# Kernel tuning notes

Measured on AMD Instinct MI355X. Metric: run time of the kernel, lower is better.

Reference implementation:

```python
import jax, jax.numpy as jnp
import numpy as np

B, S, H, NH = 2, 2048, 2048, 16
HD = H // NH  # 128
ROPE_BASE = 10000.0


def _rope(q, k, position_ids):
    # q, k: [B, NH, S, HD]; position_ids: [B, S]
    half = HD // 2
    inv_freq = 1.0 / (ROPE_BASE ** (jnp.arange(0, half, dtype=jnp.float32) / half))
    freqs = position_ids.astype(jnp.float32)[:, :, None] * inv_freq[None, None, :]  # [B,S,half]
    emb = jnp.concatenate([freqs, freqs], axis=-1)                                   # [B,S,HD]
    cos = jnp.cos(emb)[:, None, :, :]  # [B,1,S,HD]
    sin = jnp.sin(emb)[:, None, :, :]

    def rot_half(x):
        x1, x2 = jnp.split(x, 2, axis=-1)
        return jnp.concatenate([-x2, x1], axis=-1)

    q = q * cos + rot_half(q) * sin
    k = k * cos + rot_half(k) * sin
    return q, k


def setup_inputs() -> dict:
    key = jax.random.key(0)
    k1, k2, k3 = jax.random.split(key, 3)
    hidden_states = jax.random.normal(k1, (B, S, H), dtype=jnp.float32)
    position_ids = jnp.broadcast_to(jnp.arange(S, dtype=jnp.int32), (B, S))
    # additive causal mask (large finite negative to avoid inf arithmetic)
    causal = jnp.triu(jnp.full((S, S), -1e9, dtype=jnp.float32), k=1)
    attention_mask = jnp.broadcast_to(causal[None, None], (B, 1, S, S))
    qkv_w = jax.random.normal(k2, (3 * H, H), dtype=jnp.float32) * (H ** -0.5)
    qkv_b = jnp.zeros((3 * H,), dtype=jnp.float32)
    o_w = jax.random.normal(k3, (H, H), dtype=jnp.float32) * (H ** -0.5)
    return {"hidden_states": hidden_states, "position_ids": position_ids,
            "attention_mask": attention_mask, "qkv_w": qkv_w, "qkv_b": qkv_b, "o_w": o_w}


def reference(hidden_states, position_ids, attention_mask, qkv_w, qkv_b, o_w):
    qkv = hidden_states @ qkv_w.T + qkv_b                      # [B,S,3H]
    q, k, v = jnp.split(qkv, 3, axis=-1)

    def to_heads(x):
        return x.reshape(B, S, NH, HD).transpose(0, 2, 1, 3)   # [B,NH,S,HD]

    q, k, v = to_heads(q), to_heads(k), to_heads(v)
    q, k = _rope(q, k, position_ids)

    scale = 1.0 / np.sqrt(HD)
    scores = jnp.einsum('bhqd,bhkd->bhqk', q, k * scale)
    scores = scores + attention_mask
    probs = jax.nn.softmax(scores.astype(jnp.float32), axis=-1).astype(q.dtype)
    attn = jnp.einsum('bhqk,bhkd->bhqd', probs, v)
    attn = attn.transpose(0, 2, 1, 3).reshape(B, S, H)
    return attn @ o_w.T
```

## Files before the change

### kernel.cpp

```cpp
#include <hip/hip_runtime.h>
#include <hip/hip_bf16.h>

#define BB 2
#define SS 2048
#define HH 2048
#define NHH 16
#define HDD 128

using f32x4  = __attribute__((ext_vector_type(4))) float;
using bf16x8 = __attribute__((ext_vector_type(8))) short;

__device__ __forceinline__ unsigned short f2bf(float x) {
  unsigned int u = __float_as_uint(x);
  unsigned int r = (u + 0x7FFFu + ((u >> 16) & 1u)) >> 16;
  return (unsigned short)r;
}
__device__ __forceinline__ float bf2f(unsigned short u) {
  return __uint_as_float(((unsigned int)u) << 16);
}

__device__ __forceinline__ void gll16(const void* g, void* l) {
  __builtin_amdgcn_global_load_lds(
      (__attribute__((address_space(1))) void*)(g),
      (__attribute__((address_space(3))) void*)(l), 16, 0, 0);
}

#define MFMA16(a, b, c) __builtin_amdgcn_mfma_f32_16x16x32_bf16(a, b, c, 0, 0, 0)

template<int N> __device__ __forceinline__ void wlgkm() {
  static_assert(N == 0 || N == 2 || N == 4 || N == 6 || N == 8 || N == 10 || N == 12,
                "unsupported lgkmcnt");
  if constexpr (N == 0)       asm volatile("s_waitcnt lgkmcnt(0)"  ::: "memory");
  else if constexpr (N == 2)  asm volatile("s_waitcnt lgkmcnt(2)"  ::: "memory");
  else if constexpr (N == 4)  asm volatile("s_waitcnt lgkmcnt(4)"  ::: "memory");
  else if constexpr (N == 6)  asm volatile("s_waitcnt lgkmcnt(6)"  ::: "memory");
  else if constexpr (N == 8)  asm volatile("s_waitcnt lgkmcnt(8)"  ::: "memory");
  else if constexpr (N == 10) asm volatile("s_waitcnt lgkmcnt(10)" ::: "memory");
  else if constexpr (N == 12) asm volatile("s_waitcnt lgkmcnt(12)" ::: "memory");
}
template<int N> __device__ __forceinline__ void wvm() {
  static_assert(N == 0 || N == 5 || N == 6 || N == 7 || N == 8, "unsupported vmcnt");
  if constexpr (N == 0)      asm volatile("s_waitcnt vmcnt(0)" ::: "memory");
  else if constexpr (N == 5) asm volatile("s_waitcnt vmcnt(5)" ::: "memory");
  else if constexpr (N == 6) asm volatile("s_waitcnt vmcnt(6)" ::: "memory");
  else if constexpr (N == 7) asm volatile("s_waitcnt vmcnt(7)" ::: "memory");
  else if constexpr (N == 8) asm volatile("s_waitcnt vmcnt(8)" ::: "memory");
}


__global__ void convert_bf16(const float* __restrict__ in, unsigned short* __restrict__ out, int n4) {
  int i = blockIdx.x * blockDim.x + threadIdx.x;
  if (i >= n4) return;
  float4 v = reinterpret_cast<const float4*>(in)[i];
  ushort4 o;
  o.x = f2bf(v.x); o.y = f2bf(v.y); o.z = f2bf(v.z); o.w = f2bf(v.w);
  reinterpret_cast<ushort4*>(out)[i] = o;
}

__global__ void build_tab(float* __restrict__ tab) {
  int i = blockIdx.x * blockDim.x + threadIdx.x;
  if (i >= SS * 64) return;
  int s = i >> 6, j = i & 63;
  float invf = expf(-logf(10000.f) * ((float)j / 64.f));
  float a = (float)s * invf;
  tab[i * 2]     = cosf(a);
  tab[i * 2 + 1] = sinf(a);
}


template<int MODE, int MI>
__global__ __launch_bounds__(512, 1)
void gemm_pipe(const unsigned short* __restrict__ A,
               const unsigned short* __restrict__ Bw,
               const float* __restrict__ bias,
               float* __restrict__ outF,
               unsigned short* __restrict__ outQ,
               unsigned short* __restrict__ outK,
               unsigned short* __restrict__ outV,
               int Kdim) {
  constexpr int BM = 32 * MI;
  __shared__ unsigned short lA[2][BM * 64];
  __shared__ unsigned short lB[2][256 * 64];
  const int tid = threadIdx.x;
  const int tn = blockIdx.x, tm = blockIdx.y;
  const int wid = tid >> 6, lane = tid & 63;
  const int wm = wid >> 2, wn = wid & 3;
  const int lr = lane & 15, lg = lane >> 4;

  const unsigned short* Ab = A + (size_t)tm * BM * Kdim;
  const unsigned short* Bb = Bw + (size_t)tn * 256 * Kdim;

  f32x4 acc[MI][4] = {};
  bf16x8 af[MI][2], bfr[4][2];

  const int nt = Kdim >> 6;

  auto stageA = [&](int t, int h) {
    unsigned short* L = lA[t & 1];
    const int k0 = t << 6;
#pragma unroll
    for (int p = 0; p < BM / 128; ++p) {
      int cl = p * 512 + tid;
      int ri = cl >> 3, c = cl & 7;
      int row = (ri / (8 * MI)) * (16 * MI) + h * (8 * MI) + (ri % (8 * MI));
      int cg = c ^ (row & 7);
      gll16(Ab + (size_t)row * Kdim + k0 + (cg << 3), L + row * 64 + (c << 3));
    }
  };
  auto stageB = [&](int t, int h) {
    unsigned short* L = lB[t & 1];
    const int k0 = t << 6;
#pragma unroll
    for (int p = 0; p < 2; ++p) {
      int cl = p * 512 + tid;
      int ri = cl >> 3, c = cl & 7;
      int row = (ri >> 5 << 6) + (h << 5) + (ri & 31);
      int cg = c ^ (row & 7);
      gll16(Bb + (size_t)row * Kdim + k0 + (cg << 3), L + row * 64 + (c << 3));
    }
  };
  auto readAhalf = [&](int g, int h) {
    const unsigned short* la = lA[g & 1];
#pragma unroll
    for (int mi = h * (MI / 2); mi < (h + 1) * (MI / 2); ++mi) {
      int ra = wm * (BM / 2) + mi * 16 + lr;
      af[mi][0] = *reinterpret_cast<const bf16x8*>(la + ra * 64 + ((lg ^ (ra & 7)) << 3));
      af[mi][1] = *reinterpret_cast<const bf16x8*>(la + ra * 64 + (((4 + lg) ^ (ra & 7)) << 3));
    }
  };
  auto readBhalf = [&](int g, int h) {
    const unsigned short* lb = lB[g & 1];
#pragma unroll
    for (int ni = h * 2; ni < h * 2 + 2; ++ni) {
      int rb = wn * 64 + ni * 16 + lr;
      bfr[ni][0] = *reinterpret_cast<const bf16x8*>(lb + rb * 64 + ((lg ^ (rb & 7)) << 3));
      bfr[ni][1] = *reinterpret_cast<const bf16x8*>(lb + rb * 64 + (((4 + lg) ^ (rb & 7)) << 3));
    }
  };
  auto quad = [&](int ah, int bh) {
    __builtin_amdgcn_s_setprio(1);
#pragma unroll
    for (int mi = ah * (MI / 2); mi < (ah + 1) * (MI / 2); ++mi)
#pragma unroll
      for (int ni = bh * 2; ni < bh * 2 + 2; ++ni) {
        acc[mi][ni] = MFMA16(af[mi][0], bfr[ni][0], acc[mi][ni]);
        acc[mi][ni] = MFMA16(af[mi][1], bfr[ni][1], acc[mi][ni]);
      }
    __builtin_amdgcn_s_setprio(0);
  };

  stageA(0, 0); stageA(0, 1); stageB(0, 0); stageB(0, 1);
  stageA(1, 0); stageA(1, 1); stageB(1, 0); stageB(1, 1);
  if constexpr (MI == 8) wvm<8>();
  else                   wvm<6>();
  __builtin_amdgcn_s_barrier();
  __builtin_amdgcn_sched_barrier(0);
  readAhalf(0, 0);
  readBhalf(0, 0);

  for (int g = 0; g < nt; ++g) {
    readBhalf(g, 1);
    wlgkm<4>();
    __builtin_amdgcn_sched_barrier(0);
    quad(0, 0);

    readAhalf(g, 1);
    if constexpr (MI == 8) wlgkm<8>(); else wlgkm<4>();
    __builtin_amdgcn_sched_barrier(0);
    quad(0, 1);

    asm volatile("s_waitcnt vmcnt(0) lgkmcnt(0)" ::: "memory");
    __builtin_amdgcn_s_barrier();
    __builtin_amdgcn_sched_barrier(0);
    if (g + 1 < nt) readAhalf(g + 1, 0);
    if (g + 2 < nt) { stageA(g + 2, 0); stageA(g + 2, 1); }
    quad(1, 0);

    if (g + 1 < nt) readBhalf(g + 1, 0);
    if (g + 2 < nt) { stageB(g + 2, 0); stageB(g + 2, 1); }
    quad(1, 1);
  }

#pragma unroll
  for (int mi = 0; mi < MI; ++mi) {
#pragma unroll
    for (int ni = 0; ni < 4; ++ni) {
      int n = tn * 256 + wn * 64 + ni * 16 + lr;
#pragma unroll
      for (int r = 0; r < 4; ++r) {
        int m = tm * BM + wm * (BM / 2) + mi * 16 + lg * 4 + r;
        float v = acc[mi][ni][r];
        if (MODE == 1) {
          v += bias[n];
          int sel = n >> 11;
          int h = (n >> 7) & 15;
          int d = n & 127;
          int b = m >> 11;
          int s = m & 2047;
          if (sel == 0)
            outQ[(((size_t)(b * 16 + h)) * 2048 + s) * 128 + d] = f2bf(v);
          else if (sel == 1)
            outK[(((size_t)(b * 16 + h)) * 2048 + s) * 128 + d] = f2bf(v);
          else
            outV[(((size_t)(b * 16 + h)) * 128 + d) * 2048 + s] = f2bf(v);
        } else {
          outF[(size_t)m * 2048 + n] = v;
        }
      }
    }
  }
}


template<int MODE>
__global__ __launch_bounds__(256)
void gemm97(const unsigned short* __restrict__ A,
            const unsigned short* __restrict__ Bw,
            const float* __restrict__ bias,
            float* __restrict__ outF,
            unsigned short* __restrict__ outQ,
            unsigned short* __restrict__ outK,
            unsigned short* __restrict__ outV,
            int Kdim) {
  __shared__ unsigned short lA[128 * 64];
  __shared__ unsigned short lB[128 * 64];
  const int tid = threadIdx.x;
  const int tn = blockIdx.x, tm = blockIdx.y;
  const int wid = tid >> 6, lane = tid & 63;
  const int wm = wid >> 1, wn = wid & 1;
  const int lr = lane & 15, lg = lane >> 4;

  const unsigned short* Ab = A + (size_t)tm * 128 * Kdim;
  const unsigned short* Bb = Bw + (size_t)tn * 128 * Kdim;

  f32x4 acc[4][4] = {};

  const unsigned short* sa[4];
  const unsigned short* sb[4];
  unsigned short* da[4];
  unsigned short* db[4];
#pragma unroll
  for (int p = 0; p < 4; ++p) {
    int cl = p * 256 + tid;
    int ri = cl >> 3, c = cl & 7;
    int cg = c ^ (ri & 7);
    sa[p] = Ab + (size_t)ri * Kdim + (cg << 3);
    sb[p] = Bb + (size_t)ri * Kdim + (cg << 3);
    da[p] = lA + ri * 64 + (c << 3);
    db[p] = lB + ri * 64 + (c << 3);
  }

  const int nt = Kdim >> 6;

  for (int k = 0; k < nt; ++k) {
#pragma unroll
    for (int p = 0; p < 4; ++p) {
      gll16(sa[p], da[p]); sa[p] += 64;
      gll16(sb[p], db[p]); sb[p] += 64;
    }
    __syncthreads();

    bf16x8 af[4][2], bf[4][2];
#pragma unroll
    for (int t = 0; t < 4; ++t) {
      int ra = wm * 64 + t * 16 + lr;
      int rb = wn * 64 + t * 16 + lr;
      af[t][0] = *reinterpret_cast<const bf16x8*>(lA + ra * 64 + ((lg ^ (ra & 7)) << 3));
      af[t][1] = *reinterpret_cast<const bf16x8*>(lA + ra * 64 + (((4 + lg) ^ (ra & 7)) << 3));
      bf[t][0] = *reinterpret_cast<const bf16x8*>(lB + rb * 64 + ((lg ^ (rb & 7)) << 3));
      bf[t][1] = *reinterpret_cast<const bf16x8*>(lB + rb * 64 + (((4 + lg) ^ (rb & 7)) << 3));
    }
#pragma unroll
    for (int i = 0; i < 4; ++i)
#pragma unroll
      for (int j = 0; j < 4; ++j) {
        acc[i][j] = MFMA16(af[i][0], bf[j][0], acc[i][j]);
        acc[i][j] = MFMA16(af[i][1], bf[j][1], acc[i][j]);
      }
    __syncthreads();
  }

#pragma unroll
  for (int i = 0; i < 4; ++i) {
#pragma unroll
    for (int j = 0; j < 4; ++j) {
      int n = tn * 128 + wn * 64 + j * 16 + lr;
#pragma unroll
      for (int r = 0; r < 4; ++r) {
        int m = tm * 128 + wm * 64 + i * 16 + lg * 4 + r;
        float v = acc[i][j][r];
        if (MODE == 1) {
          v += bias[n];
          int sel = n >> 11;
          int h = (n >> 7) & 15;
          int d = n & 127;
          int b = m >> 11;
          int s = m & 2047;
          if (sel == 0)
            outQ[(((size_t)(b * 16 + h)) * 2048 + s) * 128 + d] = f2bf(v);
          else if (sel == 1)
            outK[(((size_t)(b * 16 + h)) * 2048 + s) * 128 + d] = f2bf(v);
          else
            outV[(((size_t)(b * 16 + h)) * 128 + d) * 2048 + s] = f2bf(v);
        } else {
          outF[(size_t)m * 2048 + n] = v;
        }
      }
    }
  }
}


__global__ void rope_inplace(unsigned short* __restrict__ Qr, unsigned short* __restrict__ Kr,
                             const int* __restrict__ pos, const float* __restrict__ tab) {
  int i = blockIdx.x * blockDim.x + threadIdx.x;
  if (i >= (1 << 20)) return;
  int jb = i & 7;
  int s  = (i >> 3) & 2047;
  int bh = (i >> 14) & 31;
  int a  = i >> 19;
  unsigned short* base = (a ? Kr : Qr) + (((size_t)bh * 2048 + s) * 128);
  int b = bh >> 4;
  int p = pos[b * 2048 + s];
  bf16x8 x1 = *reinterpret_cast<bf16x8*>(base + jb * 8);
  bf16x8 x2 = *reinterpret_cast<bf16x8*>(base + 64 + jb * 8);
  bf16x8 y1, y2;
#pragma unroll
  for (int t = 0; t < 8; ++t) {
    int j = jb * 8 + t;
    float c  = tab[((size_t)p * 64 + j) * 2];
    float sn = tab[((size_t)p * 64 + j) * 2 + 1];
    float a1 = bf2f((unsigned short)x1[t]);
    float a2 = bf2f((unsigned short)x2[t]);
    y1[t] = (short)f2bf(a1 * c - a2 * sn);
    y2[t] = (short)f2bf(a2 * c + a1 * sn);
  }
  *reinterpret_cast<bf16x8*>(base + jb * 8) = y1;
  *reinterpret_cast<bf16x8*>(base + 64 + jb * 8) = y2;
}


__global__ __launch_bounds__(256)
void attn_fwd(const unsigned short* __restrict__ Qr,
              const unsigned short* __restrict__ Kr,
              const unsigned short* __restrict__ Vt,
              unsigned short* __restrict__ attnb) {
  __shared__ unsigned short Ks[2][64 * 128];
  __shared__ unsigned short Vs[2][128 * 64];
  __shared__ unsigned short Ps[64 * 64];
  const int bx = blockIdx.x, bh = blockIdx.y;
  const int tid = threadIdx.x;
  const int wid = tid >> 6, lane = tid & 63;
  const int lr = lane & 15, lg = lane >> 4;
  const unsigned short* Qb = Qr + (size_t)bh * SS * HDD;
  const unsigned short* Kb = Kr + (size_t)bh * SS * HDD;
  const unsigned short* Vb = Vt + (size_t)bh * HDD * SS;
  const int b = bh >> 4, h = bh & 15;

  const unsigned short* ksrc0[4];
  const unsigned short* vsrc0[4];
  int dst8[4];
#pragma unroll
  for (int ch = 0; ch < 4; ++ch) {
    int c = tid + ch * 256;
    int kr = c >> 4, kc = c & 15;
    ksrc0[ch] = Kb + (size_t)kr * 128 + ((kc ^ (kr & 7)) << 3);
    int vr = c >> 3, vc = c & 7;
    vsrc0[ch] = Vb + (size_t)vr * SS + ((vc ^ (vr & 7)) << 3);
    dst8[ch] = c * 8;
  }
  const unsigned short* ksrc[4];
  const unsigned short* vsrc[4];

  auto stage = [&](int buf) {
#pragma unroll
    for (int ch = 0; ch < 4; ++ch) {
      gll16(ksrc[ch], Ks[buf] + dst8[ch]); ksrc[ch] += 64 * 128;
      gll16(vsrc[ch], Vs[buf] + dst8[ch]); vsrc[ch] += 64;
    }
  };

#pragma unroll 1
  for (int qi = 0; qi < 2; ++qi) {
    const int qt = qi ? bx : (31 - bx);

#pragma unroll
    for (int ch = 0; ch < 4; ++ch) { ksrc[ch] = ksrc0[ch]; vsrc[ch] = vsrc0[ch]; }

    bf16x8 qf[4];
#pragma unroll
    for (int kk = 0; kk < 4; ++kk)
      qf[kk] = *reinterpret_cast<const bf16x8*>(
          Qb + ((size_t)(qt * 64 + wid * 16 + lr)) * 128 + kk * 32 + lg * 8);

    f32x4 oacc[8] = {};
    float mrow[4], lsum[4];
#pragma unroll
    for (int r = 0; r < 4; ++r) { mrow[r] = -1e30f; lsum[r] = 0.f; }

    int cur = 0;
    stage(0);

#pragma unroll 1
    for (int kt = 0; kt <= qt; ++kt) {
      if (kt < qt) {
        stage(cur ^ 1);
        asm volatile("s_waitcnt vmcnt(8)" ::: "memory");
      } else {
        asm volatile("s_waitcnt vmcnt(0)" ::: "memory");
      }
      __builtin_amdgcn_s_barrier();
      __builtin_amdgcn_sched_barrier(0);

      float sv[4][4];
#pragma unroll
      for (int nt = 0; nt < 4; ++nt) {
        f32x4 sa = {};
#pragma unroll
        for (int kk = 0; kk < 4; ++kk) {
          int row = nt * 16 + lr;
          bf16x8 kf = *reinterpret_cast<const bf16x8*>(
              Ks[cur] + row * 128 + (((kk * 4 + lg) ^ (row & 7)) << 3));
          sa = __builtin_amdgcn_mfma_f32_16x16x32_bf16(qf[kk], kf, sa, 0, 0, 0);
        }
#pragma unroll
        for (int r = 0; r < 4; ++r) {
          float s = sa[r] * 0.088388347648318447f;
          if (kt == qt && (nt * 16 + lr) > (wid * 16 + lg * 4 + r)) s -= 1e9f;
          sv[nt][r] = s;
        }
      }

      float tmax[4];
#pragma unroll
      for (int r = 0; r < 4; ++r)
        tmax[r] = fmaxf(fmaxf(sv[0][r], sv[1][r]), fmaxf(sv[2][r], sv[3][r]));
#pragma unroll
      for (int r = 0; r < 4; ++r) {
        tmax[r] = fmaxf(tmax[r], __shfl_xor(tmax[r], 1));
        tmax[r] = fmaxf(tmax[r], __shfl_xor(tmax[r], 2));
        tmax[r] = fmaxf(tmax[r], __shfl_xor(tmax[r], 4));
        tmax[r] = fmaxf(tmax[r], __shfl_xor(tmax[r], 8));
      }

      float need = fmaxf(fmaxf(tmax[0] - mrow[0], tmax[1] - mrow[1]),
                         fmaxf(tmax[2] - mrow[2], tmax[3] - mrow[3]));
      if (__any(need > 8.f)) {
#pragma unroll
        for (int r = 0; r < 4; ++r) {
          float mn = fmaxf(mrow[r], tmax[r]);
          float fr = __expf(mrow[r] - mn);
          mrow[r] = mn;
          lsum[r] *= fr;
#pragma unroll
          for (int ct = 0; ct < 8; ++ct) oacc[ct][r] *= fr;
        }
      }

      float tsum[4] = {0.f, 0.f, 0.f, 0.f};
#pragma unroll
      for (int nt = 0; nt < 4; ++nt) {
        int colc = nt * 2 + (lr >> 3);
#pragma unroll
        for (int r = 0; r < 4; ++r) {
          float p = __expf(sv[nt][r] - mrow[r]);
          tsum[r] += p;
          int row = wid * 16 + lg * 4 + r;
          Ps[row * 64 + ((colc ^ (row & 7)) << 3) + (lr & 7)] = f2bf(p);
        }
      }
#pragma unroll
      for (int r = 0; r < 4; ++r) {
        tsum[r] += __shfl_xor(tsum[r], 1);
        tsum[r] += __shfl_xor(tsum[r], 2);
        tsum[r] += __shfl_xor(tsum[r], 4);
        tsum[r] += __shfl_xor(tsum[r], 8);
        lsum[r] += tsum[r];
      }

      bf16x8 pf[2];
#pragma unroll
      for (int ks = 0; ks < 2; ++ks) {
        int row = wid * 16 + lr;
        pf[ks] = *reinterpret_cast<const bf16x8*>(
            Ps + row * 64 + (((ks * 4 + lg) ^ (row & 7)) << 3));
      }
#pragma unroll
      for (int ct = 0; ct < 8; ++ct) {
#pragma unroll
        for (int ks = 0; ks < 2; ++ks) {
          int row = ct * 16 + lr;
          bf16x8 vf = *reinterpret_cast<const bf16x8*>(
              Vs[cur] + row * 64 + (((ks * 4 + lg) ^ (row & 7)) << 3));
          oacc[ct] = __builtin_amdgcn_mfma_f32_16x16x32_bf16(pf[ks], vf, oacc[ct], 0, 0, 0);
        }
      }
      __builtin_amdgcn_s_barrier();
      cur ^= 1;
    }

#pragma unroll
    for (int r = 0; r < 4; ++r) {
      float rl = 1.f / lsum[r];
      int qg = qt * 64 + wid * 16 + lg * 4 + r;
#pragma unroll
      for (int ct = 0; ct < 8; ++ct) {
        int d = ct * 16 + lr;
        attnb[((size_t)b * SS + qg) * HH + h * 128 + d] = f2bf(oacc[ct][r] * rl);
      }
    }
  }
}


extern "C" void kernel_launch(void* const* d_in, const int* in_sizes, int n_in,
                              void* d_out, int out_size, void* d_ws, size_t ws_size,
                              hipStream_t stream) {
  const float* hs     = (const float*)d_in[0];
  const int*   pos    = (const int*)d_in[1];
  const float* qkv_w  = (const float*)d_in[3];
  const float* qkv_b  = (const float*)d_in[4];
  const float* o_w    = (const float*)d_in[5];
  float* out = (float*)d_out;
  char* ws = (char*)d_ws;

  unsigned short* hsb   = (unsigned short*)(ws);
  unsigned short* wqkvb = (unsigned short*)(ws + 16777216);
  unsigned short* owb   = (unsigned short*)(ws + 41943040);
  unsigned short* Qr    = (unsigned short*)(ws + 50331648);
  unsigned short* Kr    = (unsigned short*)(ws + 67108864);
  unsigned short* Vt    = (unsigned short*)(ws + 83886080);
  unsigned short* attnb = (unsigned short*)(ws + 100663296);
  float*          tab   = (float*)(ws + 117440512);

  convert_bf16<<<2097152 / 256, 256, 0, stream>>>(hs, hsb, 2097152);
  convert_bf16<<<3145728 / 256, 256, 0, stream>>>(qkv_w, wqkvb, 3145728);
  convert_bf16<<<1048576 / 256, 256, 0, stream>>>(o_w, owb, 1048576);
  build_tab<<<512, 256, 0, stream>>>(tab);

  gemm_pipe<1, 8><<<dim3(24, 16), 512, 0, stream>>>(hsb, wqkvb, qkv_b, nullptr, Qr, Kr, Vt, 2048);
  rope_inplace<<<4096, 256, 0, stream>>>(Qr, Kr, pos, tab);
  attn_fwd<<<dim3(16, 32), 256, 0, stream>>>(Qr, Kr, Vt, attnb);
  gemm97<0><<<dim3(16, 32), 256, 0, stream>>>(attnb, owb, nullptr, out, nullptr, nullptr, nullptr, 2048);
}
```

Measured before the change: 309.9 us.

## Fuse RoPE into QKV GEMM epilogue via LDS staging; use exp2 softmax

Removes the separate rope_inplace kernel by applying the rotary embedding in the QKV GEMM epilogue. Q/K tiles are staged through swizzled shared memory so each thread can rotate matching halves and write vectorized 16-byte rows. This saves a full read/write pass over Q and K and one kernel launch. The attention softmax now folds log2(e) into the scale and uses exp2f, with the mask and rescale threshold adjusted to match; this slightly changes the epilogue's register and LDS use.

```diff
diff --git a/kernel.cpp b/kernel.cpp
--- a/kernel.cpp
+++ b/kernel.cpp
@@ -68,47 +68,45 @@
 }
 
 
-template<int MODE, int MI>
 __global__ __launch_bounds__(512, 1)
-void gemm_pipe(const unsigned short* __restrict__ A,
-               const unsigned short* __restrict__ Bw,
-               const float* __restrict__ bias,
-               float* __restrict__ outF,
-               unsigned short* __restrict__ outQ,
-               unsigned short* __restrict__ outK,
-               unsigned short* __restrict__ outV,
-               int Kdim) {
-  constexpr int BM = 32 * MI;
-  __shared__ unsigned short lA[2][BM * 64];
-  __shared__ unsigned short lB[2][256 * 64];
+void gemm_qkv(const unsigned short* __restrict__ A,
+              const unsigned short* __restrict__ Bw,
+              const float* __restrict__ bias,
+              const int* __restrict__ pos,
+              const float* __restrict__ tab,
+              unsigned short* __restrict__ outQ,
+              unsigned short* __restrict__ outK,
+              unsigned short* __restrict__ outV,
+              int Kdim) {
+  __shared__ unsigned short lds_[4][256 * 64];
   const int tid = threadIdx.x;
   const int tn = blockIdx.x, tm = blockIdx.y;
   const int wid = tid >> 6, lane = tid & 63;
   const int wm = wid >> 2, wn = wid & 3;
   const int lr = lane & 15, lg = lane >> 4;
 
-  const unsigned short* Ab = A + (size_t)tm * BM * Kdim;
+  const unsigned short* Ab = A + (size_t)tm * 256 * Kdim;
   const unsigned short* Bb = Bw + (size_t)tn * 256 * Kdim;
 
-  f32x4 acc[MI][4] = {};
-  bf16x8 af[MI][2], bfr[4][2];
+  f32x4 acc[8][4] = {};
+  bf16x8 af[8][2], bfr[4][2];
 
   const int nt = Kdim >> 6;
 
   auto stageA = [&](int t, int h) {
-    unsigned short* L = lA[t & 1];
+    unsigned short* L = lds_[t & 1];
     const int k0 = t << 6;
 #pragma unroll
-    for (int p = 0; p < BM / 128; ++p) {
+    for (int p = 0; p < 2; ++p) {
       int cl = p * 512 + tid;
       int ri = cl >> 3, c = cl & 7;
-      int row = (ri / (8 * MI)) * (16 * MI) + h * (8 * MI) + (ri % (8 * MI));
+      int row = (ri >> 6) * 128 + h * 64 + (ri & 63);
       int cg = c ^ (row & 7);
       gll16(Ab + (size_t)row * Kdim + k0 + (cg << 3), L + row * 64 + (c << 3));
     }
   };
   auto stageB = [&](int t, int h) {
-    unsigned short* L = lB[t & 1];
+    unsigned short* L = lds_[2 + (t & 1)];
     const int k0 = t << 6;
 #pragma unroll
     for (int p = 0; p < 2; ++p) {
@@ -120,16 +118,16 @@
     }
   };
   auto readAhalf = [&](int g, int h) {
-    const unsigned short* la = lA[g & 1];
-#pragma unroll
-    for (int mi = h * (MI / 2); mi < (h + 1) * (MI / 2); ++mi) {
-      int ra = wm * (BM / 2) + mi * 16 + lr;
+    const unsigned short* la = lds_[g & 1];
+#pragma unroll
+    for (int mi = h * 4; mi < h * 4 + 4; ++mi) {
+      int ra = wm * 128 + mi * 16 + lr;
       af[mi][0] = *reinterpret_cast<const bf16x8*>(la + ra * 64 + ((lg ^ (ra & 7)) << 3));
       af[mi][1] = *reinterpret_cast<const bf16x8*>(la + ra * 64 + (((4 + lg) ^ (ra & 7)) << 3));
     }
   };
   auto readBhalf = [&](int g, int h) {
-    const unsigned short* lb = lB[g & 1];
+    const unsigned short* lb = lds_[2 + (g & 1)];
 #pragma unroll
     for (int ni = h * 2; ni < h * 2 + 2; ++ni) {
       int rb = wn * 64 + ni * 16 + lr;
@@ -140,7 +138,7 @@
   auto quad = [&](int ah, int bh) {
     __builtin_amdgcn_s_setprio(1);
 #pragma unroll
-    for (int mi = ah * (MI / 2); mi < (ah + 1) * (MI / 2); ++mi)
+    for (int mi = ah * 4; mi < ah * 4 + 4; ++mi)
 #pragma unroll
       for (int ni = bh * 2; ni < bh * 2 + 2; ++ni) {
         acc[mi][ni] = MFMA16(af[mi][0], bfr[ni][0], acc[mi][ni]);
@@ -151,8 +149,7 @@
 
   stageA(0, 0); stageA(0, 1); stageB(0, 0); stageB(0, 1);
   stageA(1, 0); stageA(1, 1); stageB(1, 0); stageB(1, 1);
-  if constexpr (MI == 8) wvm<8>();
-  else                   wvm<6>();
+  wvm<8>();
   __builtin_amdgcn_s_barrier();
   __builtin_amdgcn_sched_barrier(0);
   readAhalf(0, 0);
@@ -165,7 +162,7 @@
     quad(0, 0);
 
     readAhalf(g, 1);
-    if constexpr (MI == 8) wlgkm<8>(); else wlgkm<4>();
+    wlgkm<8>();
     __builtin_amdgcn_sched_barrier(0);
     quad(0, 1);
 
@@ -181,30 +178,74 @@
     quad(1, 1);
   }
 
-#pragma unroll
-  for (int mi = 0; mi < MI; ++mi) {
-#pragma unroll
-    for (int ni = 0; ni < 4; ++ni) {
-      int n = tn * 256 + wn * 64 + ni * 16 + lr;
-#pragma unroll
-      for (int r = 0; r < 4; ++r) {
-        int m = tm * BM + wm * (BM / 2) + mi * 16 + lg * 4 + r;
-        float v = acc[mi][ni][r];
-        if (MODE == 1) {
-          v += bias[n];
-          int sel = n >> 11;
-          int h = (n >> 7) & 15;
-          int d = n & 127;
+  if (tn < 16) {
+    unsigned short* Ls = &lds_[0][0];
+    __syncthreads();
+#pragma unroll
+    for (int mi = 0; mi < 8; ++mi) {
+#pragma unroll
+      for (int ni = 0; ni < 4; ++ni) {
+        int n_l = wn * 64 + ni * 16 + lr;
+        float bv = bias[tn * 256 + n_l];
+#pragma unroll
+        for (int r = 0; r < 4; ++r) {
+          int m_l = wm * 128 + mi * 16 + lg * 4 + r;
+          Ls[m_l * 256 + (n_l ^ ((m_l & 7) << 3))] = f2bf(acc[mi][ni][r] + bv);
+        }
+      }
+    }
+    __syncthreads();
+
+    unsigned short* outX = (tn < 8) ? outQ : outK;
+    const int jb = (tid & 7) * 8;
+    const int r0 = (tid >> 3) * 4;
+#pragma unroll
+    for (int rr = 0; rr < 4; ++rr) {
+      int row = r0 + rr;
+      int m = tm * 256 + row;
+      int b = m >> 11, s = m & 2047;
+      int p = pos[b * 2048 + s];
+      float cs[8], sn[8];
+#pragma unroll
+      for (int j = 0; j < 8; ++j) {
+        float2 t2 = *reinterpret_cast<const float2*>(&tab[((size_t)p * 64 + jb + j) * 2]);
+        cs[j] = t2.x; sn[j] = t2.y;
+      }
+      int swz = (row & 7) << 3;
+#pragma unroll
+      for (int hb = 0; hb < 2; ++hb) {
+        bf16x8 x1 = *reinterpret_cast<const bf16x8*>(&Ls[row * 256 + (hb * 128 + (jb ^ swz))]);
+        bf16x8 x2 = *reinterpret_cast<const bf16x8*>(&Ls[row * 256 + (hb * 128 + 64 + (jb ^ swz))]);
+        bf16x8 y1, y2;
+#pragma unroll
+        for (int j = 0; j < 8; ++j) {
+          float a1 = bf2f((unsigned short)x1[j]);
+          float a2 = bf2f((unsigned short)x2[j]);
+          y1[j] = (short)f2bf(a1 * cs[j] - a2 * sn[j]);
+          y2[j] = (short)f2bf(a2 * cs[j] + a1 * sn[j]);
+        }
+        int n0 = tn * 256 + hb * 128;
+        int h = (n0 >> 7) & 15;
+        unsigned short* dst = outX + (((size_t)(b * 16 + h)) * 2048 + s) * 128;
+        *reinterpret_cast<bf16x8*>(&dst[jb]) = y1;
+        *reinterpret_cast<bf16x8*>(&dst[64 + jb]) = y2;
+      }
+    }
+  } else {
+#pragma unroll
+    for (int mi = 0; mi < 8; ++mi) {
+#pragma unroll
+      for (int ni = 0; ni < 4; ++ni) {
+        int n = tn * 256 + wn * 64 + ni * 16 + lr;
+        float bv = bias[n];
+        int h = (n >> 7) & 15;
+        int d = n & 127;
+#pragma unroll
+        for (int r = 0; r < 4; ++r) {
+          int m = tm * 256 + wm * 128 + mi * 16 + lg * 4 + r;
           int b = m >> 11;
           int s = m & 2047;
-          if (sel == 0)
-            outQ[(((size_t)(b * 16 + h)) * 2048 + s) * 128 + d] = f2bf(v);
-          else if (sel == 1)
-            outK[(((size_t)(b * 16 + h)) * 2048 + s) * 128 + d] = f2bf(v);
-          else
-            outV[(((size_t)(b * 16 + h)) * 128 + d) * 2048 + s] = f2bf(v);
-        } else {
-          outF[(size_t)m * 2048 + n] = v;
+          outV[(((size_t)(b * 16 + h)) * 128 + d) * 2048 + s] = f2bf(acc[mi][ni][r] + bv);
         }
       }
     }
@@ -216,11 +257,7 @@
 __global__ __launch_bounds__(256)
 void gemm97(const unsigned short* __restrict__ A,
             const unsigned short* __restrict__ Bw,
-            const float* __restrict__ bias,
             float* __restrict__ outF,
-            unsigned short* __restrict__ outQ,
-            unsigned short* __restrict__ outK,
-            unsigned short* __restrict__ outV,
             int Kdim) {
   __shared__ unsigned short lA[128 * 64];
   __shared__ unsigned short lB[128 * 64];
@@ -288,55 +325,10 @@
 #pragma unroll
       for (int r = 0; r < 4; ++r) {
         int m = tm * 128 + wm * 64 + i * 16 + lg * 4 + r;
-        float v = acc[i][j][r];
-        if (MODE == 1) {
-          v += bias[n];
-          int sel = n >> 11;
-          int h = (n >> 7) & 15;
-          int d = n & 127;
-          int b = m >> 11;
-          int s = m & 2047;
-          if (sel == 0)
-            outQ[(((size_t)(b * 16 + h)) * 2048 + s) * 128 + d] = f2bf(v);
-          else if (sel == 1)
-            outK[(((size_t)(b * 16 + h)) * 2048 + s) * 128 + d] = f2bf(v);
-          else
-            outV[(((size_t)(b * 16 + h)) * 128 + d) * 2048 + s] = f2bf(v);
-        } else {
-          outF[(size_t)m * 2048 + n] = v;
-        }
-      }
-    }
-  }
-}
-
-
-__global__ void rope_inplace(unsigned short* __restrict__ Qr, unsigned short* __restrict__ Kr,
-                             const int* __restrict__ pos, const float* __restrict__ tab) {
-  int i = blockIdx.x * blockDim.x + threadIdx.x;
-  if (i >= (1 << 20)) return;
-  int jb = i & 7;
-  int s  = (i >> 3) & 2047;
-  int bh = (i >> 14) & 31;
-  int a  = i >> 19;
-  unsigned short* base = (a ? Kr : Qr) + (((size_t)bh * 2048 + s) * 128);
-  int b = bh >> 4;
-  int p = pos[b * 2048 + s];
-  bf16x8 x1 = *reinterpret_cast<bf16x8*>(base + jb * 8);
-  bf16x8 x2 = *reinterpret_cast<bf16x8*>(base + 64 + jb * 8);
-  bf16x8 y1, y2;
-#pragma unroll
-  for (int t = 0; t < 8; ++t) {
-    int j = jb * 8 + t;
-    float c  = tab[((size_t)p * 64 + j) * 2];
-    float sn = tab[((size_t)p * 64 + j) * 2 + 1];
-    float a1 = bf2f((unsigned short)x1[t]);
-    float a2 = bf2f((unsigned short)x2[t]);
-    y1[t] = (short)f2bf(a1 * c - a2 * sn);
-    y2[t] = (short)f2bf(a2 * c + a1 * sn);
-  }
-  *reinterpret_cast<bf16x8*>(base + jb * 8) = y1;
-  *reinterpret_cast<bf16x8*>(base + 64 + jb * 8) = y2;
+        outF[(size_t)m * 2048 + n] = acc[i][j][r];
+      }
+    }
+  }
 }
 
 
@@ -356,6 +348,7 @@
   const unsigned short* Kb = Kr + (size_t)bh * SS * HDD;
   const unsigned short* Vb = Vt + (size_t)bh * HDD * SS;
   const int b = bh >> 4, h = bh & 15;
+  const float SC2 = 0.12751763f;
 
   const unsigned short* ksrc0[4];
   const unsigned short* vsrc0[4];
@@ -425,8 +418,8 @@
         }
 #pragma unroll
         for (int r = 0; r < 4; ++r) {
-          float s = sa[r] * 0.088388347648318447f;
-          if (kt == qt && (nt * 16 + lr) > (wid * 16 + lg * 4 + r)) s -= 1e9f;
+          float s = sa[r] * SC2;
+          if (kt == qt && (nt * 16 + lr) > (wid * 16 + lg * 4 + r)) s -= 1.5e9f;
           sv[nt][r] = s;
         }
       }
@@ -445,11 +438,11 @@
 
       float need = fmaxf(fmaxf(tmax[0] - mrow[0], tmax[1] - mrow[1]),
                          fmaxf(tmax[2] - mrow[2], tmax[3] - mrow[3]));
-      if (__any(need > 8.f)) {
+      if (__any(need > 11.54f)) {
 #pragma unroll
         for (int r = 0; r < 4; ++r) {
           float mn = fmaxf(mrow[r], tmax[r]);
-          float fr = __expf(mrow[r] - mn);
+          float fr = exp2f(mrow[r] - mn);
           mrow[r] = mn;
           lsum[r] *= fr;
 #pragma unroll
@@ -463,7 +456,7 @@
         int colc = nt * 2 + (lr >> 3);
 #pragma unroll
         for (int r = 0; r < 4; ++r) {
-          float p = __expf(sv[nt][r] - mrow[r]);
+          float p = exp2f(sv[nt][r] - mrow[r]);
           tsum[r] += p;
           int row = wid * 16 + lg * 4 + r;
           Ps[row * 64 + ((colc ^ (row & 7)) << 3) + (lr & 7)] = f2bf(p);
@@ -538,8 +531,7 @@
   convert_bf16<<<1048576 / 256, 256, 0, stream>>>(o_w, owb, 1048576);
   build_tab<<<512, 256, 0, stream>>>(tab);
 
-  gemm_pipe<1, 8><<<dim3(24, 16), 512, 0, stream>>>(hsb, wqkvb, qkv_b, nullptr, Qr, Kr, Vt, 2048);
-  rope_inplace<<<4096, 256, 0, stream>>>(Qr, Kr, pos, tab);
+  gemm_qkv<<<dim3(24, 16), 512, 0, stream>>>(hsb, wqkvb, qkv_b, pos, tab, Qr, Kr, Vt, 2048);
   attn_fwd<<<dim3(16, 32), 256, 0, stream>>>(Qr, Kr, Vt, attnb);
-  gemm97<0><<<dim3(16, 32), 256, 0, stream>>>(attnb, owb, nullptr, out, nullptr, nullptr, nullptr, 2048);
-}
+  gemm97<0><<<dim3(16, 32), 256, 0, stream>>>(attnb, owb, out, 2048);
+}
```

Result: faster. 281.4 us (-9.2%).
